# Performance work log

Hardware: AMD Instinct MI355X
Metric: run time of the kernel (lower is better)

Reference implementation:

```python
import jax, jax.numpy as jnp
import numpy as np
from jax import lax

B, C, IMG, P = 64, 3, 256, 16
D, K, NC, NH = 128, 512, 8, 4
GRID = IMG // P
N = GRID * GRID  # 256 patches
HD = D // NH


def setup_inputs() -> dict:
    key = jax.random.key(0)
    ks = jax.random.split(key, 16)
    s = 0.02
    f32 = jnp.float32
    return {
        'image': jax.random.uniform(ks[0], (B, C, IMG, IMG), f32),
        'conv_w': jax.random.normal(ks[1], (D, C, P, P), f32) * s,
        'conv_b': jnp.zeros((D,), f32),
        'stat_w1': jax.random.normal(ks[2], (128, 15), f32) * s,
        'stat_b1': jnp.zeros((128,), f32),
        'stat_w2': jax.random.normal(ks[3], (D, 128), f32) * s,
        'stat_b2': jnp.zeros((D,), f32),
        'pos_embed': jax.random.normal(ks[4], (1, N, D), f32) * s,
        'ln1_s': jnp.ones((2, D), f32), 'ln1_b': jnp.zeros((2, D), f32),
        'qkv_w': jax.random.normal(ks[5], (2, 3 * D, D), f32) * s,
        'qkv_b': jnp.zeros((2, 3 * D), f32),
        'out_w': jax.random.normal(ks[6], (2, D, D), f32) * s,
        'out_b': jnp.zeros((2, D), f32),
        'ln2_s': jnp.ones((2, D), f32), 'ln2_b': jnp.zeros((2, D), f32),
        'ff1_w': jax.random.normal(ks[7], (2, 2 * D, D), f32) * s,
        'ff1_b': jnp.zeros((2, 2 * D), f32),
        'ff2_w': jax.random.normal(ks[8], (2, D, 2 * D), f32) * s,
        'ff2_b': jnp.zeros((2, D), f32),
        'codebook': jax.random.uniform(ks[9], (K, D), f32, -1.0 / K, 1.0 / K),
        'head_w': jax.random.normal(ks[10], (NC, D), f32) * s,
        'head_b': jnp.zeros((NC,), f32),
    }


def _ln(x, s, b, eps=1e-5):
    mu = x.mean(-1, keepdims=True)
    var = jnp.var(x, axis=-1, keepdims=True)
    return (x - mu) / jnp.sqrt(var + eps) * s + b


def _stats(image):
    # mean/std(unbiased)/min/max per channel + skew/kurt/dark of luminance -> 15 feats
    px = image.reshape(B, C, -1)
    mean = px.mean(-1)
    std = px.std(-1, ddof=1)
    mn = px.min(-1)
    mx = px.max(-1)
    lum = 0.299 * px[:, 0] + 0.587 * px[:, 1] + 0.114 * px[:, 2]
    cen = lum - lum.mean(-1, keepdims=True)
    sd = lum.std(-1)  # biased, matches unbiased=False
    skew = (cen ** 3).mean(-1) / (sd ** 3 + 1e-6)
    kurt = (cen ** 4).mean(-1) / (sd ** 4 + 1e-6)
    dark = (lum < 0.2).astype(jnp.float32).mean(-1)
    return jnp.concatenate([mean, std, mn, mx, skew[:, None], kurt[:, None], dark[:, None]], -1)


def _forward(image, conv_w, conv_b, stat_w1, stat_b1, stat_w2, stat_b2, pos_embed,
             ln1_s, ln1_b, qkv_w, qkv_b, out_w, out_b, ln2_s, ln2_b,
             ff1_w, ff1_b, ff2_w, ff2_b, codebook, head_w, head_b):
    # patch embedding: non-overlapping conv, stride = kernel = P
    patch = lax.conv_general_dilated(image, conv_w, (P, P), 'VALID',
                                     dimension_numbers=('NCHW', 'OIHW', 'NCHW'))
    patch = (patch + conv_b[None, :, None, None]).reshape(B, D, N).transpose(0, 2, 1)  # (B,N,D)
    # statistical encoder (eval: dropout off)
    sf = jax.nn.relu(_stats(image) @ stat_w1.T + stat_b1) @ stat_w2.T + stat_b2  # (B,D)
    x = patch + pos_embed + sf[:, None, :]
    # 2-layer pre-LN transformer encoder
    for i in range(2):
        h = _ln(x, ln1_s[i], ln1_b[i])
        qkv = h @ qkv_w[i].T + qkv_b[i]
        q, k, v = jnp.split(qkv, 3, axis=-1)
        q = q.reshape(B, N, NH, HD).transpose(0, 2, 1, 3)
        k = k.reshape(B, N, NH, HD).transpose(0, 2, 1, 3)
        v = v.reshape(B, N, NH, HD).transpose(0, 2, 1, 3)
        attn = jax.nn.softmax(jnp.einsum('bhqd,bhkd->bhqk', q, k) / jnp.sqrt(jnp.float32(HD)), -1)
        o = jnp.einsum('bhqk,bhkd->bhqd', attn, v).transpose(0, 2, 1, 3).reshape(B, N, D)
        x = x + o @ out_w[i].T + out_b[i]
        h = _ln(x, ln2_s[i], ln2_b[i])
        x = x + jax.nn.gelu(h @ ff1_w[i].T + ff1_b[i], approximate=False) @ ff2_w[i].T + ff2_b[i]
    # VQ: nearest-codebook lookup with straight-through estimator
    zf = x.reshape(-1, D)
    dist = (zf * zf).sum(1, keepdims=True) + (codebook * codebook).sum(1) - 2.0 * (zf @ codebook.T)
    idx = jnp.argmin(dist, axis=1)  # (B*N,)
    qz = codebook[idx].reshape(B, N, D)
    quant = x + lax.stop_gradient(qz - x)
    counts = jnp.zeros((K,), jnp.float32).at[idx].add(1.0)
    p = counts / idx.size
    perplexity = jnp.exp(-jnp.sum(p * jnp.log(p + 1e-10)))
    gf = quant.mean(1)
    logits = gf @ head_w.T + head_b
    return quant, idx.reshape(B, N), logits, gf, perplexity


def reference(image, conv_w, conv_b, stat_w1, stat_b1, stat_w2, stat_b2, pos_embed,
              ln1_s, ln1_b, qkv_w, qkv_b, out_w, out_b, ln2_s, ln2_b,
              ff1_w, ff1_b, ff2_w, ff2_b, codebook, head_w, head_b):
    return _forward(image, conv_w, conv_b, stat_w1, stat_b1, stat_w2, stat_b2, pos_embed,
                    ln1_s, ln1_b, qkv_w, qkv_b, out_w, out_b, ln2_s, ln2_b,
                    ff1_w, ff1_b, ff2_w, ff2_b, codebook, head_w, head_b)
```

## Files before the change

kernel.cpp:

```cpp
#include <hip/hip_runtime.h>
#include <math.h>

__device__ __forceinline__ void gload16(const float* g, float* l) {
    __builtin_amdgcn_global_load_lds(
        (const __attribute__((address_space(1))) void*)g,
        (__attribute__((address_space(3))) void*)l, 16, 0, 0);
}

__device__ __forceinline__ double wred_add(double v) {
    #pragma unroll
    for (int o = 32; o > 0; o >>= 1) v += __shfl_xor(v, o);
    return v;
}
__device__ __forceinline__ float wred_min(float v) {
    #pragma unroll
    for (int o = 32; o > 0; o >>= 1) v = fminf(v, __shfl_xor(v, o));
    return v;
}
__device__ __forceinline__ float wred_max(float v) {
    #pragma unroll
    for (int o = 32; o > 0; o >>= 1) v = fmaxf(v, __shfl_xor(v, o));
    return v;
}

#define PREC 17

__global__ __launch_bounds__(256) void stats_partial_kernel(const float* __restrict__ img,
                                                            double* __restrict__ part)
{
    int b = blockIdx.x >> 5, blk = blockIdx.x & 31;
    int tid = threadIdx.x;
    const float* r0 = img + (size_t)b * 3 * 65536;
    const float* g0 = r0 + 65536;
    const float* b0 = r0 + 131072;
    int base = blk*2048 + tid*8;
    double s0=0,s1=0,s2=0,q0=0,q1=0,q2=0,l1=0,l2=0,l3=0,l4=0,dark=0;
    float mn0=1e30f,mn1=1e30f,mn2=1e30f, mx0=-1e30f,mx1=-1e30f,mx2=-1e30f;
    #pragma unroll
    for (int u = 0; u < 2; ++u) {
        float4 rv = *(const float4*)&r0[base + u*4];
        float4 gv = *(const float4*)&g0[base + u*4];
        float4 bv = *(const float4*)&b0[base + u*4];
        float rr[4] = {rv.x, rv.y, rv.z, rv.w};
        float gg[4] = {gv.x, gv.y, gv.z, gv.w};
        float bbv[4] = {bv.x, bv.y, bv.z, bv.w};
        #pragma unroll
        for (int e = 0; e < 4; ++e) {
            float r = rr[e], g = gg[e], bl = bbv[e];
            double rd_ = r, gd = g, bd = bl;
            s0 += rd_; q0 += rd_*rd_; mn0 = fminf(mn0, r); mx0 = fmaxf(mx0, r);
            s1 += gd;  q1 += gd*gd;   mn1 = fminf(mn1, g); mx1 = fmaxf(mx1, g);
            s2 += bd;  q2 += bd*bd;   mn2 = fminf(mn2, bl); mx2 = fmaxf(mx2, bl);
            double lum = 0.299*rd_ + 0.587*gd + 0.114*bd;
            double d2 = lum*lum;
            l1 += lum; l2 += d2; l3 += d2*lum; l4 += d2*d2;
            if (lum < 0.2) dark += 1.0;
        }
    }
    double dv[11] = {s0,s1,s2,q0,q1,q2,l1,l2,l3,l4,dark};
    #pragma unroll
    for (int q = 0; q < 11; ++q) dv[q] = wred_add(dv[q]);
    mn0 = wred_min(mn0); mn1 = wred_min(mn1); mn2 = wred_min(mn2);
    mx0 = wred_max(mx0); mx1 = wred_max(mx1); mx2 = wred_max(mx2);
    __shared__ double sd[4][PREC];
    int w = tid >> 6, lane = tid & 63;
    if (lane == 0) {
        #pragma unroll
        for (int q = 0; q < 11; ++q) sd[w][q] = dv[q];
        sd[w][11] = (double)mn0; sd[w][12] = (double)mn1; sd[w][13] = (double)mn2;
        sd[w][14] = (double)mx0; sd[w][15] = (double)mx1; sd[w][16] = (double)mx2;
    }
    __syncthreads();
    if (tid == 0) {
        double out[PREC];
        #pragma unroll
        for (int q = 0; q < PREC; ++q) out[q] = sd[0][q];
        #pragma unroll
        for (int ww = 1; ww < 4; ++ww) {
            #pragma unroll
            for (int q = 0; q < 11; ++q) out[q] += sd[ww][q];
            out[11] = fmin(out[11], sd[ww][11]); out[12] = fmin(out[12], sd[ww][12]);
            out[13] = fmin(out[13], sd[ww][13]);
            out[14] = fmax(out[14], sd[ww][14]); out[15] = fmax(out[15], sd[ww][15]);
            out[16] = fmax(out[16], sd[ww][16]);
        }
        double* p = part + (size_t)(b*32 + blk)*PREC;
        #pragma unroll
        for (int q = 0; q < PREC; ++q) p[q] = out[q];
    }
}

__global__ __launch_bounds__(32) void stats_final_kernel(const double* __restrict__ part,
                                                         double* __restrict__ feats)
{
    int b = blockIdx.x, t = threadIdx.x;
    const double* p = part + (size_t)(b*32 + t)*PREC;
    double v[PREC];
    #pragma unroll
    for (int q = 0; q < PREC; ++q) v[q] = p[q];
    #pragma unroll
    for (int o = 16; o > 0; o >>= 1) {
        #pragma unroll
        for (int q = 0; q < 11; ++q) v[q] += __shfl_xor(v[q], o);
        #pragma unroll
        for (int q = 11; q < 14; ++q) v[q] = fmin(v[q], __shfl_xor(v[q], o));
        #pragma unroll
        for (int q = 14; q < PREC; ++q) v[q] = fmax(v[q], __shfl_xor(v[q], o));
    }
    if (t == 0) {
        const double n = 65536.0;
        double* f = feats + b*15;
        for (int c = 0; c < 3; ++c) {
            double su = v[c], sq = v[3+c];
            f[c]   = su/n;
            f[3+c] = sqrt((sq - su*su/n) / (n - 1.0));
            f[6+c] = v[11+c];
            f[9+c] = v[14+c];
        }
        double m1 = v[6]/n, m2 = v[7]/n, m3 = v[8]/n, m4 = v[9]/n;
        double mu2 = m2 - m1*m1;
        double mu3 = m3 - 3.0*m1*m2 + 2.0*m1*m1*m1;
        double mu4 = m4 - 4.0*m1*m3 + 6.0*m1*m1*m2 - 3.0*m1*m1*m1*m1;
        double sd = sqrt(mu2);
        f[12] = mu3 / (sd*sd*sd + 1e-6);
        f[13] = mu4 / (sd*sd*sd*sd + 1e-6);
        f[14] = v[10] / n;
    }
}

__global__ __launch_bounds__(128) void sfmlp_kernel(const double* __restrict__ feats,
    const float* __restrict__ w1, const float* __restrict__ b1,
    const float* __restrict__ w2, const float* __restrict__ b2,
    double* __restrict__ sf)
{
    int b = blockIdx.x, t = threadIdx.x;
    __shared__ double fs[15];
    __shared__ double hs[128];
    if (t < 15) fs[t] = feats[b*15 + t];
    __syncthreads();
    double h = (double)b1[t];
    for (int j = 0; j < 15; ++j) h += fs[j] * (double)w1[t*15 + j];
    hs[t] = fmax(h, 0.0);
    __syncthreads();
    double o = (double)b2[t];
    for (int j = 0; j < 128; ++j) o += hs[j] * (double)w2[t*128 + j];
    sf[b*128 + t] = o;
}

__device__ __forceinline__ int swz64(int r, int kq4) {
    return r*64 + (((kq4) ^ (r & 15)) << 2);
}

__global__ __launch_bounds__(256) void patch_sk_kernel(const float* __restrict__ img,
    const float* __restrict__ w, float* __restrict__ Pa, float* __restrict__ Pb4)
{
    __shared__ float As[4096];
    __shared__ float Ws[4096];
    int tid = threadIdx.x;
    int tx = tid & 15, ty = tid >> 4;
    int m0 = blockIdx.x * 64, n0 = blockIdx.y * 64;
    int z = blockIdx.z;
    int kbase = z * 192;
    int wv = tid >> 6;
    float acc[4][4] = {};
    for (int k0 = 0; k0 < 192; k0 += 64) {
        #pragma unroll
        for (int call = 0; call < 4; ++call) {
            int s = call*256 + tid;
            int row = s >> 4, kq = (s & 15) ^ (row & 15);
            int m = m0 + row;
            int bb = m >> 8, pat = m & 255;
            int gy = pat >> 4, gx = pat & 15;
            int k = kbase + k0 + kq*4;
            int c = k >> 8, rem = k & 255;
            int py = rem >> 4, px = rem & 15;
            gload16(&img[(size_t)(bb*3 + c)*65536 + (size_t)(gy*16+py)*256 + gx*16 + px],
                    As + (call*256 + wv*64)*4);
            gload16(&w[(size_t)(n0+row)*768 + k], Ws + (call*256 + wv*64)*4);
        }
        __syncthreads();
        #pragma unroll 8
        for (int q = 0; q < 16; ++q) {
            float4 a4[4], w4[4];
            #pragma unroll
            for (int i=0;i<4;++i) a4[i] = *(const float4*)&As[swz64(ty + 16*i, q)];
            #pragma unroll
            for (int j=0;j<4;++j) w4[j] = *(const float4*)&Ws[swz64(tx + 16*j, q)];
            #pragma unroll
            for (int i=0;i<4;++i)
                #pragma unroll
                for (int j=0;j<4;++j) {
                    acc[i][j] = fmaf(a4[i].x, w4[j].x, acc[i][j]);
                    acc[i][j] = fmaf(a4[i].y, w4[j].y, acc[i][j]);
                    acc[i][j] = fmaf(a4[i].z, w4[j].z, acc[i][j]);
                    acc[i][j] = fmaf(a4[i].w, w4[j].w, acc[i][j]);
                }
        }
        __syncthreads();
    }
    float* P = (z < 3) ? (Pa + (size_t)z*2097152) : Pb4;
    #pragma unroll
    for (int i=0;i<4;++i){
        int m = m0 + ty + 16*i;
        #pragma unroll
        for (int j=0;j<4;++j){
            int n = n0 + tx + 16*j;
            P[(size_t)m*128 + n] = acc[i][j];
        }
    }
}

__global__ __launch_bounds__(256) void gemm_kernel(const float* __restrict__ A, int lda,
    const float* __restrict__ W, const float* __restrict__ bias,
    float* __restrict__ C, int M, int N, int K, int epi)
{
    __shared__ float As[4096];
    __shared__ float Ws[4096];
    int tid = threadIdx.x;
    int tx = tid & 15, ty = tid >> 4;
    int m0 = blockIdx.x * 64, n0 = blockIdx.y * 64;
    int wv = tid >> 6;
    float acc[4][4] = {};
    for (int k0 = 0; k0 < K; k0 += 64) {
        #pragma unroll
        for (int call = 0; call < 4; ++call) {
            int s = call*256 + tid;
            int row = s >> 4, kq = (s & 15) ^ (row & 15);
            gload16(&A[(size_t)(m0+row)*lda + k0 + kq*4], As + (call*256 + wv*64)*4);
            gload16(&W[(size_t)(n0+row)*K + k0 + kq*4], Ws + (call*256 + wv*64)*4);
        }
        __syncthreads();
        #pragma unroll 8
        for (int q = 0; q < 16; ++q) {
            float4 a4[4], w4[4];
            #pragma unroll
            for (int i=0;i<4;++i) a4[i] = *(const float4*)&As[swz64(ty + 16*i, q)];
            #pragma unroll
            for (int j=0;j<4;++j) w4[j] = *(const float4*)&Ws[swz64(tx + 16*j, q)];
            #pragma unroll
            for (int i=0;i<4;++i)
                #pragma unroll
                for (int j=0;j<4;++j) {
                    acc[i][j] = fmaf(a4[i].x, w4[j].x, acc[i][j]);
                    acc[i][j] = fmaf(a4[i].y, w4[j].y, acc[i][j]);
                    acc[i][j] = fmaf(a4[i].z, w4[j].z, acc[i][j]);
                    acc[i][j] = fmaf(a4[i].w, w4[j].w, acc[i][j]);
                }
        }
        __syncthreads();
    }
    #pragma unroll
    for (int i=0;i<4;++i){
        int m = m0 + ty + 16*i;
        #pragma unroll
        for (int j=0;j<4;++j){
            int n = n0 + tx + 16*j;
            float v = acc[i][j] + bias[n];
            if (epi == 0) {
                C[(size_t)m*N + n] = v;
            } else {
                C[(size_t)m*N + n] = 0.5f*v*(1.0f + erff(v*0.70710678118654752f));
            }
        }
    }
}

__global__ __launch_bounds__(256) void gemm_sk_kernel(const float* __restrict__ A, int lda,
    const float* __restrict__ W, int K, int K2,
    float* __restrict__ P0, float* __restrict__ P1, int ldo)
{
    __shared__ float As[4096];
    __shared__ float Ws[4096];
    int tid = threadIdx.x;
    int tx = tid & 15, ty = tid >> 4;
    int m0 = blockIdx.x * 64, n0 = blockIdx.y * 64;
    int kbase = blockIdx.z * K2;
    int wv = tid >> 6;
    float acc[4][4] = {};
    for (int k0 = 0; k0 < K2; k0 += 64) {
        #pragma unroll
        for (int call = 0; call < 4; ++call) {
            int s = call*256 + tid;
            int row = s >> 4, kq = (s & 15) ^ (row & 15);
            gload16(&A[(size_t)(m0+row)*lda + kbase + k0 + kq*4], As + (call*256 + wv*64)*4);
            gload16(&W[(size_t)(n0+row)*K + kbase + k0 + kq*4], Ws + (call*256 + wv*64)*4);
        }
        __syncthreads();
        #pragma unroll 8
        for (int q = 0; q < 16; ++q) {
            float4 a4[4], w4[4];
            #pragma unroll
            for (int i=0;i<4;++i) a4[i] = *(const float4*)&As[swz64(ty + 16*i, q)];
            #pragma unroll
            for (int j=0;j<4;++j) w4[j] = *(const float4*)&Ws[swz64(tx + 16*j, q)];
            #pragma unroll
            for (int i=0;i<4;++i)
                #pragma unroll
                for (int j=0;j<4;++j) {
                    acc[i][j] = fmaf(a4[i].x, w4[j].x, acc[i][j]);
                    acc[i][j] = fmaf(a4[i].y, w4[j].y, acc[i][j]);
                    acc[i][j] = fmaf(a4[i].z, w4[j].z, acc[i][j]);
                    acc[i][j] = fmaf(a4[i].w, w4[j].w, acc[i][j]);
                }
        }
        __syncthreads();
    }
    float* P = blockIdx.z ? P1 : P0;
    #pragma unroll
    for (int i=0;i<4;++i){
        int m = m0 + ty + 16*i;
        #pragma unroll
        for (int j=0;j<4;++j){
            int n = n0 + tx + 16*j;
            P[(size_t)m*ldo + n] = acc[i][j];
        }
    }
}

__global__ __launch_bounds__(256) void cpatch_kernel(const float* __restrict__ pa,
    const float* __restrict__ p3, const float* __restrict__ bias,
    const float* __restrict__ pos, const double* __restrict__ sf,
    const float* __restrict__ ls, const float* __restrict__ lb,
    float* __restrict__ x, float* __restrict__ h)
{
    int tid = threadIdx.x;
    int lane = tid & 63, w = tid >> 6;
    int row = blockIdx.x*4 + w;
    int bb = row >> 8, pat = row & 255;
    int n = lane*2;
    float2 a0 = *(const float2*)&pa[(size_t)row*128 + n];
    float2 a1 = *(const float2*)&pa[2097152 + (size_t)row*128 + n];
    float2 a2 = *(const float2*)&pa[4194304 + (size_t)row*128 + n];
    float2 a3 = *(const float2*)&p3[(size_t)row*128 + n];
    float v0 = ((a0.x + a1.x) + a2.x) + a3.x + bias[n]   + pos[pat*128 + n]   + (float)sf[bb*128 + n];
    float v1 = ((a0.y + a1.y) + a2.y) + a3.y + bias[n+1] + pos[pat*128 + n+1] + (float)sf[bb*128 + n+1];
    *(float2*)&x[(size_t)row*128 + n] = make_float2(v0, v1);
    double v0d = v0, v1d = v1;
    double sum = v0d + v1d, sq = v0d*v0d + v1d*v1d;
    #pragma unroll
    for (int o = 32; o > 0; o >>= 1) { sum += __shfl_xor(sum, o); sq += __shfl_xor(sq, o); }
    double mean = sum * (1.0/128.0);
    double var  = sq  * (1.0/128.0) - mean*mean;
    double inv  = 1.0 / sqrt(var + 1e-5);
    float2 o2;
    o2.x = (float)((v0d - mean)*inv*(double)ls[n]   + (double)lb[n]);
    o2.y = (float)((v1d - mean)*inv*(double)ls[n+1] + (double)lb[n+1]);
    *(float2*)&h[(size_t)row*128 + n] = o2;
}

__global__ __launch_bounds__(256) void cres_kernel(float* __restrict__ x,
    const float* __restrict__ p0, int ld0, const float* __restrict__ p1, int ld1,
    const float* __restrict__ bias,
    const float* __restrict__ ls, const float* __restrict__ lb,
    float* __restrict__ h, int doLN)
{
    int tid = threadIdx.x;
    int lane = tid & 63, w = tid >> 6;
    int row = blockIdx.x*4 + w;
    int n = lane*2;
    float2 a0 = *(const float2*)&p0[(size_t)row*ld0 + n];
    float2 a1 = *(const float2*)&p1[(size_t)row*ld1 + n];
    float2 xv = *(const float2*)&x[(size_t)row*128 + n];
    float v0 = xv.x + (a0.x + a1.x + bias[n]);
    float v1 = xv.y + (a0.y + a1.y + bias[n+1]);
    *(float2*)&x[(size_t)row*128 + n] = make_float2(v0, v1);
    if (doLN) {
        double v0d = v0, v1d = v1;
        double sum = v0d + v1d, sq = v0d*v0d + v1d*v1d;
        #pragma unroll
        for (int o = 32; o > 0; o >>= 1) { sum += __shfl_xor(sum, o); sq += __shfl_xor(sq, o); }
        double mean = sum * (1.0/128.0);
        double var  = sq  * (1.0/128.0) - mean*mean;
        double inv  = 1.0 / sqrt(var + 1e-5);
        float2 o2;
        o2.x = (float)((v0d - mean)*inv*(double)ls[n]   + (double)lb[n]);
        o2.y = (float)((v1d - mean)*inv*(double)ls[n+1] + (double)lb[n+1]);
        *(float2*)&h[(size_t)row*128 + n] = o2;
    }
}

__global__ __launch_bounds__(512, 4) void attn_kernel(float* __restrict__ qkv)
{
    __shared__ float Ks[256*36];
    __shared__ float Vs[256*36];
    int tid = threadIdx.x;
    int b = blockIdx.x >> 3, h = (blockIdx.x >> 1) & 3, half = blockIdx.x & 1;
    {
        int row = tid >> 1, p16 = (tid & 1) * 16;
        size_t rb = (size_t)(b*256 + row) * 384;
        const float* kp = qkv + rb + 128 + h*32 + p16;
        const float* vp = qkv + rb + 256 + h*32 + p16;
        #pragma unroll
        for (int i = 0; i < 4; ++i) {
            *(float4*)&Ks[row*36 + p16 + i*4] = *(const float4*)&kp[i*4];
            *(float4*)&Vs[row*36 + p16 + i*4] = *(const float4*)&vp[i*4];
        }
    }
    int qrow = half*128 + (tid >> 2);
    int ds = (tid >> 1) & 1;
    int ks = tid & 1;
    const float scale = 0.17677669529663687f;
    float q[16];
    const float* qp = qkv + (size_t)(b*256 + qrow)*384 + h*32 + ds*16;
    #pragma unroll
    for (int i = 0; i < 16; ++i) q[i] = qp[i] * scale;
    __syncthreads();
    float o[16];
    #pragma unroll
    for (int i = 0; i < 16; ++i) o[i] = 0.f;
    float l = 0.f;
    for (int it = 0; it < 128; ++it) {
        int j = it*2 + ks;
        const float* kr = &Ks[j*36 + ds*16];
        float s = 0.f;
        #pragma unroll
        for (int i = 0; i < 16; ++i) s = fmaf(q[i], kr[i], s);
        s += __shfl_xor(s, 2);
        float e = __expf(s);
        l += e;
        const float* vr = &Vs[j*36 + ds*16];
        #pragma unroll
        for (int i = 0; i < 16; ++i) o[i] = fmaf(e, vr[i], o[i]);
    }
    l += __shfl_xor(l, 1);
    #pragma unroll
    for (int i = 0; i < 16; ++i) o[i] += __shfl_xor(o[i], 1);
    if (ks == 0) {
        float inv = 1.0f / l;
        float* op = qkv + (size_t)(b*256 + qrow)*384 + h*32 + ds*16;
        #pragma unroll
        for (int i = 0; i < 16; ++i) op[i] = o[i] * inv;
    }
}

__global__ __launch_bounds__(256) void cc_kernel(const float* __restrict__ cb,
                                                 float* __restrict__ ccs)
{
    int c = blockIdx.x*256 + threadIdx.x;
    const float* p = cb + (size_t)c*128;
    float r[8];
    #pragma unroll
    for (int j = 0; j < 8; ++j) { float v = p[j]; r[j] = v*v; }
    for (int i = 8; i < 128; i += 8)
        #pragma unroll
        for (int j = 0; j < 8; ++j) { float v = p[i+j]; r[j] += v*v; }
    ccs[c] = ((r[0]+r[1]) + (r[2]+r[3])) + ((r[4]+r[5]) + (r[6]+r[7]));
}

#define ZC(k) (((k)&3)==0 ? z[(k)>>2].x : ((k)&3)==1 ? z[(k)>>2].y : ((k)&3)==2 ? z[(k)>>2].z : z[(k)>>2].w)

__global__ __launch_bounds__(128) void vq_dist_kernel(const float* __restrict__ x,
    const float* __restrict__ cb, const float* __restrict__ ccs,
    float* __restrict__ pbv, int* __restrict__ pbi)
{
    __shared__ float Cs[8192];
    __shared__ float ccl[64];
    int tid = threadIdx.x;
    int m = blockIdx.x*128 + tid;
    int split = blockIdx.y;
    int cbase = split*64;
    const float4* cbp = (const float4*)(cb + (size_t)cbase*128);
    for (int e = tid; e < 2048; e += 128) ((float4*)Cs)[e] = cbp[e];
    if (tid < 64) ccl[tid] = ccs[cbase + tid];
    float4 z[32];
    const float4* zp = (const float4*)(x + (size_t)m*128);
    #pragma unroll
    for (int i = 0; i < 32; ++i) z[i] = zp[i];
    float r[8];
    #pragma unroll
    for (int j = 0; j < 8; ++j) { float v = ZC(j); r[j] = v*v; }
    #pragma unroll
    for (int i = 8; i < 128; i += 8)
        #pragma unroll
        for (int j = 0; j < 8; ++j) { float v = ZC(i+j); r[j] += v*v; }
    float zz = ((r[0]+r[1]) + (r[2]+r[3])) + ((r[4]+r[5]) + (r[6]+r[7]));
    __syncthreads();
    float bestv = INFINITY;
    int   besti = 0;
    for (int g = 0; g < 16; ++g) {
        const float* c0 = &Cs[(g*4+0)*128];
        const float* c1 = &Cs[(g*4+1)*128];
        const float* c2 = &Cs[(g*4+2)*128];
        const float* c3 = &Cs[(g*4+3)*128];
        float a0 = 0.f, a1 = 0.f, a2 = 0.f, a3 = 0.f;
        #pragma unroll
        for (int q = 0; q < 32; ++q) {
            float4 v0 = *(const float4*)&c0[q*4];
            float4 v1 = *(const float4*)&c1[q*4];
            float4 v2 = *(const float4*)&c2[q*4];
            float4 v3 = *(const float4*)&c3[q*4];
            float4 zq = z[q];
            a0 = fmaf(zq.x, v0.x, a0); a0 = fmaf(zq.y, v0.y, a0);
            a0 = fmaf(zq.z, v0.z, a0); a0 = fmaf(zq.w, v0.w, a0);
            a1 = fmaf(zq.x, v1.x, a1); a1 = fmaf(zq.y, v1.y, a1);
            a1 = fmaf(zq.z, v1.z, a1); a1 = fmaf(zq.w, v1.w, a1);
            a2 = fmaf(zq.x, v2.x, a2); a2 = fmaf(zq.y, v2.y, a2);
            a2 = fmaf(zq.z, v2.z, a2); a2 = fmaf(zq.w, v2.w, a2);
            a3 = fmaf(zq.x, v3.x, a3); a3 = fmaf(zq.y, v3.y, a3);
            a3 = fmaf(zq.z, v3.z, a3); a3 = fmaf(zq.w, v3.w, a3);
        }
        int code = cbase + g*4;
        float t1, d;
        t1 = zz + ccl[g*4+0]; d = t1 - 2.0f*a0; if (d < bestv) { bestv = d; besti = code;   }
        t1 = zz + ccl[g*4+1]; d = t1 - 2.0f*a1; if (d < bestv) { bestv = d; besti = code+1; }
        t1 = zz + ccl[g*4+2]; d = t1 - 2.0f*a2; if (d < bestv) { bestv = d; besti = code+2; }
        t1 = zz + ccl[g*4+3]; d = t1 - 2.0f*a3; if (d < bestv) { bestv = d; besti = code+3; }
    }
    pbv[(size_t)split*16384 + m] = bestv;
    pbi[(size_t)split*16384 + m] = besti;
}

__global__ __launch_bounds__(256) void vq_merge_kernel(const float* __restrict__ pbv,
    const int* __restrict__ pbi, const float* __restrict__ cb,
    float* __restrict__ quant, float* __restrict__ idxf, float* __restrict__ counts)
{
    __shared__ int fidx[32];
    int tid = threadIdx.x;
    int m0 = blockIdx.x*32;
    if (tid < 32) {
        int m = m0 + tid;
        float v = pbv[m]; int gi = pbi[m];
        #pragma unroll
        for (int s = 1; s < 8; ++s) {
            float vv = pbv[(size_t)s*16384 + m]; int ii = pbi[(size_t)s*16384 + m];
            if (vv < v) { v = vv; gi = ii; }
        }
        fidx[tid] = gi;
        idxf[m] = (float)gi;
        atomicAdd(&counts[gi], 1.0f);
    }
    __syncthreads();
    #pragma unroll
    for (int e0 = 0; e0 < 4; ++e0) {
        int e = e0*256 + tid;
        int rr = e >> 5, k4 = e & 31;
        ((float4*)&quant[(size_t)(m0+rr)*128])[k4] = ((const float4*)&cb[(size_t)fidx[rr]*128])[k4];
    }
}

__global__ __launch_bounds__(128) void gf_logits_kernel(const float* __restrict__ quant,
    const float* __restrict__ head_w, const float* __restrict__ head_b,
    float* __restrict__ gf, float* __restrict__ logits)
{
    int b = blockIdx.x, d = threadIdx.x;
    double s = 0.0;
    for (int n = 0; n < 256; ++n) s += (double)quant[(size_t)(b*256+n)*128 + d];
    double g = s * (1.0/256.0);
    gf[b*128 + d] = (float)g;
    __shared__ double gs[128];
    gs[d] = g;
    __syncthreads();
    if (d < 8) {
        double l = (double)head_b[d];
        for (int k = 0; k < 128; ++k) l += gs[k] * (double)head_w[d*128 + k];
        logits[b*8 + d] = (float)l;
    }
}

__global__ __launch_bounds__(512) void perp_kernel(const float* __restrict__ counts,
                                                   float* __restrict__ out)
{
    __shared__ double sh[512];
    int t = threadIdx.x;
    double p = (double)counts[t] * (1.0/16384.0);
    sh[t] = p * log(p + 1e-10);
    __syncthreads();
    for (int s = 256; s > 0; s >>= 1) { if (t < s) sh[t] += sh[t+s]; __syncthreads(); }
    if (t == 0) out[0] = (float)exp(-sh[0]);
}

extern "C" void kernel_launch(void* const* d_in, const int* in_sizes, int n_in,
                              void* d_out, int out_size, void* d_ws, size_t ws_size,
                              hipStream_t stream)
{
    const float* image   = (const float*)d_in[0];
    const float* conv_w  = (const float*)d_in[1];
    const float* conv_b  = (const float*)d_in[2];
    const float* stat_w1 = (const float*)d_in[3];
    const float* stat_b1 = (const float*)d_in[4];
    const float* stat_w2 = (const float*)d_in[5];
    const float* stat_b2 = (const float*)d_in[6];
    const float* pos     = (const float*)d_in[7];
    const float* ln1_s   = (const float*)d_in[8];
    const float* ln1_b   = (const float*)d_in[9];
    const float* qkv_w   = (const float*)d_in[10];
    const float* qkv_b   = (const float*)d_in[11];
    const float* out_w   = (const float*)d_in[12];
    const float* out_b   = (const float*)d_in[13];
    const float* ln2_s   = (const float*)d_in[14];
    const float* ln2_b   = (const float*)d_in[15];
    const float* ff1_w   = (const float*)d_in[16];
    const float* ff1_b   = (const float*)d_in[17];
    const float* ff2_w   = (const float*)d_in[18];
    const float* ff2_b   = (const float*)d_in[19];
    const float* codebook= (const float*)d_in[20];
    const float* head_w  = (const float*)d_in[21];
    const float* head_b  = (const float*)d_in[22];

    char* wsb = (char*)d_ws;
    float*  x32   = (float*) (wsb);
    float*  h32   = (float*) (wsb + 8388608);
    float*  qkv32 = (float*) (wsb + 16777216);
    double* sf64  = (double*)(wsb + 41943040);
    double* feats = (double*)(wsb + 42008576);
    float*  counts= (float*) (wsb + 42016256);
    double* part  = (double*)(wsb + 42018304);
    float*  pbv   = (float*) (wsb + 42296832);
    int*    pbi   = (int*)   (wsb + 42821120);
    float*  ccs   = (float*) (wsb + 43345408);

    float* outf   = (float*)d_out;
    float* quant  = outf;
    float* idxf   = quant + 2097152;
    float* logits = idxf + 16384;
    float* gf     = logits + 512;
    float* perp   = gf + 8192;

    hipMemsetAsync(counts, 0, 512*sizeof(float), stream);

    stats_partial_kernel<<<2048, 256, 0, stream>>>(image, part);
    stats_final_kernel<<<64, 32, 0, stream>>>(part, feats);
    sfmlp_kernel<<<64, 128, 0, stream>>>(feats, stat_w1, stat_b1, stat_w2, stat_b2, sf64);
    cc_kernel<<<2, 256, 0, stream>>>(codebook, ccs);

    patch_sk_kernel<<<dim3(256, 2, 4), 256, 0, stream>>>(image, conv_w, qkv32, h32);
    cpatch_kernel<<<4096, 256, 0, stream>>>(qkv32, h32, conv_b, pos, sf64,
                                            ln1_s, ln1_b, x32, h32);

    for (int i = 0; i < 2; ++i) {
        gemm_kernel<<<dim3(256, 6), 256, 0, stream>>>(h32, 128, qkv_w + (size_t)i*384*128,
                                                      qkv_b + i*384, qkv32, 16384, 384, 128, 0);
        attn_kernel<<<512, 512, 0, stream>>>(qkv32);
        gemm_sk_kernel<<<dim3(256, 2, 2), 256, 0, stream>>>(qkv32, 384,
                                                            out_w + (size_t)i*128*128, 128, 64,
                                                            qkv32 + 128, qkv32 + 256, 384);
        cres_kernel<<<4096, 256, 0, stream>>>(x32, qkv32 + 128, 384, qkv32 + 256, 384,
                                              out_b + i*128, ln2_s + i*128, ln2_b + i*128,
                                              h32, 1);
        gemm_kernel<<<dim3(256, 4), 256, 0, stream>>>(h32, 128, ff1_w + (size_t)i*256*128,
                                                      ff1_b + i*256, qkv32, 16384, 256, 128, 2);
        gemm_sk_kernel<<<dim3(256, 2, 2), 256, 0, stream>>>(qkv32, 256,
                                                            ff2_w + (size_t)i*128*256, 256, 128,
                                                            qkv32 + 4194304, h32, 128);
        cres_kernel<<<4096, 256, 0, stream>>>(x32, qkv32 + 4194304, 128, h32, 128,
                                              ff2_b + i*128, ln1_s + 128, ln1_b + 128,
                                              h32, i == 0 ? 1 : 0);
    }

    vq_dist_kernel<<<dim3(128, 8), 128, 0, stream>>>(x32, codebook, ccs, pbv, pbi);
    vq_merge_kernel<<<512, 256, 0, stream>>>(pbv, pbi, codebook, quant, idxf, counts);
    gf_logits_kernel<<<64, 128, 0, stream>>>(quant, head_w, head_b, gf, logits);
    perp_kernel<<<1, 512, 0, stream>>>(counts, perp);
}
```

Measured before the change: 501.5 us.

## Restructure attention to one thread per query row, one block per (batch, head)

The attention kernel now assigns a whole query row (all 32 head dims, all 256 keys) to a single thread, with one 256-thread block per batch-head instead of two 512-thread blocks splitting queries, dims and keys. This removes the cross-lane shuffles for partial dot products and output reduction, and halves K/V shared-memory loading per head. In exchange it launches only 256 blocks of 256 threads, which cuts parallelism sharply and raises register pressure with 32-wide q/o arrays.

Measured after the change: 525.3 us. 4.7% more time.

```diff
diff --git a/kernel.cpp b/kernel.cpp
--- a/kernel.cpp
+++ b/kernel.cpp
@@ -379,58 +379,52 @@
     }
 }
 
-__global__ __launch_bounds__(512, 4) void attn_kernel(float* __restrict__ qkv)
+__global__ __launch_bounds__(256, 2) void attn_kernel(float* __restrict__ qkv)
 {
     __shared__ float Ks[256*36];
     __shared__ float Vs[256*36];
     int tid = threadIdx.x;
-    int b = blockIdx.x >> 3, h = (blockIdx.x >> 1) & 3, half = blockIdx.x & 1;
+    int b = blockIdx.x >> 2, h = blockIdx.x & 3;
+    const float scale = 0.17677669529663687f;
+    size_t rb = (size_t)(b*256 + tid) * 384;
     {
-        int row = tid >> 1, p16 = (tid & 1) * 16;
-        size_t rb = (size_t)(b*256 + row) * 384;
-        const float* kp = qkv + rb + 128 + h*32 + p16;
-        const float* vp = qkv + rb + 256 + h*32 + p16;
-        #pragma unroll
-        for (int i = 0; i < 4; ++i) {
-            *(float4*)&Ks[row*36 + p16 + i*4] = *(const float4*)&kp[i*4];
-            *(float4*)&Vs[row*36 + p16 + i*4] = *(const float4*)&vp[i*4];
-        }
-    }
-    int qrow = half*128 + (tid >> 2);
-    int ds = (tid >> 1) & 1;
-    int ks = tid & 1;
-    const float scale = 0.17677669529663687f;
-    float q[16];
-    const float* qp = qkv + (size_t)(b*256 + qrow)*384 + h*32 + ds*16;
-    #pragma unroll
-    for (int i = 0; i < 16; ++i) q[i] = qp[i] * scale;
-    __syncthreads();
-    float o[16];
-    #pragma unroll
-    for (int i = 0; i < 16; ++i) o[i] = 0.f;
+        const float* kp = qkv + rb + 128 + h*32;
+        const float* vp = qkv + rb + 256 + h*32;
+        #pragma unroll
+        for (int i = 0; i < 8; ++i) {
+            *(float4*)&Ks[tid*36 + i*4] = *(const float4*)&kp[i*4];
+            *(float4*)&Vs[tid*36 + i*4] = *(const float4*)&vp[i*4];
+        }
+    }
+    float q[32];
+    const float* qp = qkv + rb + h*32;
+    #pragma unroll
+    for (int i = 0; i < 32; ++i) q[i] = qp[i] * scale;
+    __syncthreads();
+    float o[32];
+    #pragma unroll
+    for (int i = 0; i < 32; ++i) o[i] = 0.f;
     float l = 0.f;
-    for (int it = 0; it < 128; ++it) {
-        int j = it*2 + ks;
-        const float* kr = &Ks[j*36 + ds*16];
-        float s = 0.f;
-        #pragma unroll
-        for (int i = 0; i < 16; ++i) s = fmaf(q[i], kr[i], s);
-        s += __shfl_xor(s, 2);
-        float e = __expf(s);
+    for (int j = 0; j < 256; ++j) {
+        const float* kr = &Ks[j*36];
+        float s0 = 0.f, s1 = 0.f, s2 = 0.f, s3 = 0.f;
+        #pragma unroll
+        for (int i = 0; i < 8; ++i) {
+            s0 = fmaf(q[i],    kr[i],    s0);
+            s1 = fmaf(q[8+i],  kr[8+i],  s1);
+            s2 = fmaf(q[16+i], kr[16+i], s2);
+            s3 = fmaf(q[24+i], kr[24+i], s3);
+        }
+        float e = __expf((s0 + s1) + (s2 + s3));
         l += e;
-        const float* vr = &Vs[j*36 + ds*16];
-        #pragma unroll
-        for (int i = 0; i < 16; ++i) o[i] = fmaf(e, vr[i], o[i]);
-    }
-    l += __shfl_xor(l, 1);
-    #pragma unroll
-    for (int i = 0; i < 16; ++i) o[i] += __shfl_xor(o[i], 1);
-    if (ks == 0) {
-        float inv = 1.0f / l;
-        float* op = qkv + (size_t)(b*256 + qrow)*384 + h*32 + ds*16;
-        #pragma unroll
-        for (int i = 0; i < 16; ++i) op[i] = o[i] * inv;
-    }
+        const float* vr = &Vs[j*36];
+        #pragma unroll
+        for (int i = 0; i < 32; ++i) o[i] = fmaf(e, vr[i], o[i]);
+    }
+    float inv = 1.0f / l;
+    float* op = qkv + rb + h*32;
+    #pragma unroll
+    for (int i = 0; i < 32; ++i) op[i] = o[i] * inv;
 }
 
 __global__ __launch_bounds__(256) void cc_kernel(const float* __restrict__ cb,
@@ -630,7 +624,7 @@
     for (int i = 0; i < 2; ++i) {
         gemm_kernel<<<dim3(256, 6), 256, 0, stream>>>(h32, 128, qkv_w + (size_t)i*384*128,
                                                       qkv_b + i*384, qkv32, 16384, 384, 128, 0);
-        attn_kernel<<<512, 512, 0, stream>>>(qkv32);
+        attn_kernel<<<256, 256, 0, stream>>>(qkv32);
         gemm_sk_kernel<<<dim3(256, 2, 2), 256, 0, stream>>>(qkv32, 384,
                                                             out_w + (size_t)i*128*128, 128, 64,
                                                             qkv32 + 128, qkv32 + 256, 384);
```
